# Kernel tuning notes

Hardware: AMD Instinct MI355X
Metric: run time of the kernel (lower is better)

Reference implementation:

```python
import jax, jax.numpy as jnp
import numpy as np

N, E, D = 100000, 1280000, 64


def setup_inputs() -> dict:
    key = jax.random.key(0)
    ks = jax.random.split(key, 9)
    x = jax.random.normal(ks[0], (N, D), jnp.float32)
    edge_index = jax.random.randint(ks[1], (2, E), 0, N, dtype=jnp.int64)
    edge_weight = jax.random.uniform(ks[2], (E,), jnp.float32)
    s = 1.0 / np.sqrt(D)
    W0 = jax.random.normal(ks[3], (D, D), jnp.float32) * s
    b0 = jnp.zeros((D,), jnp.float32)
    W1 = jax.random.normal(ks[4], (D, D), jnp.float32) * s
    b1 = jnp.zeros((D,), jnp.float32)
    W2 = jax.random.normal(ks[5], (D, D), jnp.float32) * s
    b2 = jnp.zeros((D,), jnp.float32)
    return {"x": x, "edge_index": edge_index, "edge_weight": edge_weight,
            "W0": W0, "b0": b0, "W1": W1, "b1": b1, "W2": W2, "b2": b2}


def reference(x, edge_index, edge_weight, W0, b0, W1, b1, W2, b2):
    n = x.shape[0]
    row, col = edge_index[0], edge_index[1]
    # GCN normalization with self-loops (PyG gcn_norm, fill_value=1)
    loop = jnp.arange(n)
    row_f = jnp.concatenate([row, loop])
    col_f = jnp.concatenate([col, loop])
    w_f = jnp.concatenate([edge_weight, jnp.ones((n,), x.dtype)])
    deg = jax.ops.segment_sum(w_f, col_f, num_segments=n)
    dinv = jnp.where(deg > 0, jax.lax.rsqrt(deg), 0.0).astype(x.dtype)
    norm = dinv[row_f] * w_f * dinv[col_f]  # [E+N]

    def conv(h, W, b):
        h = h @ W                                  # [N, D_out]
        msg = h[row_f] * norm[:, None]             # gather + scale
        return jax.ops.segment_sum(msg, col_f, num_segments=n) + b

    results = [x]
    h = jax.nn.relu(conv(x, W0, b0))   # dropout p=0 / eval -> identity
    results.append(h)
    h = jax.nn.relu(conv(h, W1, b1))
    results.append(h)
    h = conv(h, W2, b2)                # last layer: no activation
    results.append(h)
    return tuple(results)
```

## Files before the change

kernel.cpp:

```cpp
#include <hip/hip_runtime.h>
#include <hip/hip_fp16.h>


#define TPB 256
#define P1_CHUNK 4096
#define DSH 7
#define DNB 128
#define STAGE_CAP 4096

__global__ __launch_bounds__(TPB) void k_p0(const int* __restrict__ col,
                                            int* __restrict__ chist, int E, int nbk) {
    __shared__ int h[1024];
    int tid = threadIdx.x;
    for (int i = tid; i < nbk; i += TPB) h[i] = 0;
    __syncthreads();
    int s0 = blockIdx.x * P1_CHUNK;
    int s1 = min(s0 + P1_CHUNK, E);
    for (int i = s0 + tid; i < s1; i += TPB) atomicAdd(&h[col[i] >> DSH], 1);
    __syncthreads();
    for (int i = tid; i < nbk; i += TPB)
        if (h[i]) atomicAdd(&chist[i], h[i]);
}

__global__ __launch_bounds__(1024) void k_scanb(const int* __restrict__ chist,
                                                int* __restrict__ cbase,
                                                int* __restrict__ ccur, int nbk, int E) {
    __shared__ int s[1024];
    int tid = threadIdx.x;
    int v = (tid < nbk) ? chist[tid] : 0;
    s[tid] = v;
    __syncthreads();
    for (int off = 1; off < 1024; off <<= 1) {
        int t = (tid >= off) ? s[tid - off] : 0;
        __syncthreads();
        s[tid] += t;
        __syncthreads();
    }
    if (tid < nbk) { int ex = s[tid] - v; cbase[tid] = ex; ccur[tid] = ex; }
    if (tid == 0) cbase[nbk] = E;
}

__global__ __launch_bounds__(TPB) void k_p1(const int* __restrict__ row,
                                            const int* __restrict__ col,
                                            const float* __restrict__ w,
                                            int* __restrict__ ccur,
                                            int2* __restrict__ bkt, int E, int nbk) {
    __shared__ int h[1024];
    __shared__ int base[1024];
    int tid = threadIdx.x;
    for (int i = tid; i < nbk; i += TPB) h[i] = 0;
    __syncthreads();
    int s0 = blockIdx.x * P1_CHUNK;
    int s1 = min(s0 + P1_CHUNK, E);
    for (int i = s0 + tid; i < s1; i += TPB) atomicAdd(&h[col[i] >> DSH], 1);
    __syncthreads();
    for (int i = tid; i < nbk; i += TPB) {
        int c = h[i];
        base[i] = c ? atomicAdd(&ccur[i], c) : 0;
        h[i] = 0;
    }
    __syncthreads();
    for (int i = s0 + tid; i < s1; i += TPB) {
        int c = col[i];
        int b = c >> DSH;
        int r = atomicAdd(&h[b], 1);
        bkt[base[b] + r] = make_int2(row[i] | ((c & (DNB - 1)) << 20), __float_as_int(w[i]));
    }
}

__global__ __launch_bounds__(TPB) void k_p2(const int2* __restrict__ bkt,
                                            const int* __restrict__ cbase,
                                            int* __restrict__ starts,
                                            int2* __restrict__ edges,
                                            float* __restrict__ dinv, int n, int E) {
    __shared__ int hist[DNB];
    __shared__ int curs[DNB];
    __shared__ int sc[DNB];
    __shared__ int2 stage[STAGE_CAP];
    int tid = threadIdx.x;
    int b = blockIdx.x;
    int s0 = cbase[b], s1 = cbase[b + 1];
    int cnt = s1 - s0;
    int nodeBase = b << DSH;
    if (tid < DNB) hist[tid] = 0;
    __syncthreads();
    for (int i = s0 + tid; i < s1; i += TPB)
        atomicAdd(&hist[(unsigned)bkt[i].x >> 20], 1);
    __syncthreads();
    int v = 0;
    if (tid < DNB) { v = hist[tid]; sc[tid] = v; }
    __syncthreads();
    for (int off = 1; off < DNB; off <<= 1) {
        int t = 0;
        if (tid < DNB && tid >= off) t = sc[tid - off];
        __syncthreads();
        if (tid < DNB) sc[tid] += t;
        __syncthreads();
    }
    if (tid < DNB) {
        int ex = sc[tid] - v;
        curs[tid] = ex;
        int node = nodeBase + tid;
        if (node < n) starts[node] = s0 + ex;
    }
    if (b == 0 && tid == 0) starts[n] = E;
    __syncthreads();
    if (cnt <= STAGE_CAP) {
        for (int i = s0 + tid; i < s1; i += TPB) {
            int2 ed = bkt[i];
            int d = (unsigned)ed.x >> 20;
            int r = atomicAdd(&curs[d], 1);
            stage[r] = make_int2(ed.x & 0xFFFFF, ed.y);
        }
        __syncthreads();
        for (int i = tid; i < cnt; i += TPB) edges[s0 + i] = stage[i];
        if (tid < DNB) {
            int node = nodeBase + tid;
            if (node < n) {
                float d = 1.0f;
                for (int j = sc[tid] - v; j < sc[tid]; ++j)
                    d += __int_as_float(stage[j].y);
                dinv[node] = rsqrtf(d);
            }
        }
    } else {
        for (int i = s0 + tid; i < s1; i += TPB) {
            int2 ed = bkt[i];
            int d = (unsigned)ed.x >> 20;
            int r = atomicAdd(&curs[d], 1);
            edges[s0 + r] = make_int2(ed.x & 0xFFFFF, ed.y);
        }
        __syncthreads();
        if (tid < DNB) {
            int node = nodeBase + tid;
            if (node < n) {
                float d = 1.0f;
                for (int j = sc[tid] - v; j < sc[tid]; ++j)
                    d += __int_as_float(edges[s0 + j].y);
                dinv[node] = rsqrtf(d);
            }
        }
    }
}

__global__ __launch_bounds__(TPB, 3) void k_gemm64(const float* __restrict__ in,
                                                   const float* __restrict__ Wg,
                                                   __half* __restrict__ hwh,
                                                   const float* __restrict__ dinvg,
                                                   float* __restrict__ cp, int n) {
    __shared__ float4 Ws[1024];
    __shared__ float4 As[2048];
    int tid = threadIdx.x;
    const float4* Wf4 = (const float4*)Wg;
    #pragma unroll
    for (int i = 0; i < 4; ++i) Ws[i * 256 + tid] = Wf4[i * 256 + tid];
    int rowbase = blockIdx.x * 128;
    const float4* Af4 = (const float4*)in;
    #pragma unroll
    for (int i = 0; i < 8; ++i) {
        int f4 = i * 256 + tid;
        int r = f4 >> 4, c4 = f4 & 15;
        float4 v = make_float4(0.f, 0.f, 0.f, 0.f);
        if (rowbase + r < n) {
            v = Af4[(size_t)(rowbase + r) * 16 + c4];
            if (cp) *(float4*)&cp[((size_t)(rowbase + r) * 16 + c4) * 4] = v;
        }
        As[r * 16 + (c4 ^ ((r >> 3) & 3))] = v;
    }
    __syncthreads();
    int jg = tid & 15;
    int rg = tid >> 4;
    int r0 = rg * 8;
    int sw = rg & 3;
    float4 acc[8];
    #pragma unroll
    for (int rr = 0; rr < 8; ++rr) acc[rr] = make_float4(0.f, 0.f, 0.f, 0.f);
    #pragma unroll 2
    for (int kt = 0; kt < 16; ++kt) {
        float4 w0 = Ws[(kt * 4 + 0) * 16 + jg];
        float4 w1 = Ws[(kt * 4 + 1) * 16 + jg];
        float4 w2 = Ws[(kt * 4 + 2) * 16 + jg];
        float4 w3 = Ws[(kt * 4 + 3) * 16 + jg];
        int ac = kt ^ sw;
        #pragma unroll
        for (int rr = 0; rr < 8; ++rr) {
            float4 a = As[(r0 + rr) * 16 + ac];
            acc[rr].x = fmaf(a.x, w0.x, acc[rr].x);
            acc[rr].y = fmaf(a.x, w0.y, acc[rr].y);
            acc[rr].z = fmaf(a.x, w0.z, acc[rr].z);
            acc[rr].w = fmaf(a.x, w0.w, acc[rr].w);
            acc[rr].x = fmaf(a.y, w1.x, acc[rr].x);
            acc[rr].y = fmaf(a.y, w1.y, acc[rr].y);
            acc[rr].z = fmaf(a.y, w1.z, acc[rr].z);
            acc[rr].w = fmaf(a.y, w1.w, acc[rr].w);
            acc[rr].x = fmaf(a.z, w2.x, acc[rr].x);
            acc[rr].y = fmaf(a.z, w2.y, acc[rr].y);
            acc[rr].z = fmaf(a.z, w2.z, acc[rr].z);
            acc[rr].w = fmaf(a.z, w2.w, acc[rr].w);
            acc[rr].x = fmaf(a.w, w3.x, acc[rr].x);
            acc[rr].y = fmaf(a.w, w3.y, acc[rr].y);
            acc[rr].z = fmaf(a.w, w3.z, acc[rr].z);
            acc[rr].w = fmaf(a.w, w3.w, acc[rr].w);
        }
    }
    #pragma unroll
    for (int rr = 0; rr < 8; ++rr) {
        int r = rowbase + r0 + rr;
        if (r < n) {
            float di = dinvg[r];
            ushort4 s;
            s.x = __half_as_ushort(__float2half(acc[rr].x * di));
            s.y = __half_as_ushort(__float2half(acc[rr].y * di));
            s.z = __half_as_ushort(__float2half(acc[rr].z * di));
            s.w = __half_as_ushort(__float2half(acc[rr].w * di));
            *(ushort4*)&hwh[(size_t)r * 64 + jg * 4] = s;
        }
    }
}

__global__ __launch_bounds__(TPB) void k_gather(const int* __restrict__ starts,
                                                const int2* __restrict__ edges,
                                                const __half* __restrict__ hwh,
                                                const float* __restrict__ dinv,
                                                const float* __restrict__ b,
                                                float* __restrict__ out,
                                                int n, int relu) {
    int node = blockIdx.x * 4 + (threadIdx.x >> 6);
    if (node >= n) return;
    int lane = threadIdx.x & 63;
    int eslot = lane >> 4;
    int f = (lane & 15) << 2;
    int s0 = starts[node], s1 = starts[node + 1];
    float4 acc = make_float4(0.f, 0.f, 0.f, 0.f);
    const long long* epk = (const long long*)edges;
    int e = s0 + eslot;
    for (; e + 4 < s1; e += 8) {
        long long ev0 = __builtin_nontemporal_load(&epk[e]);
        long long ev1 = __builtin_nontemporal_load(&epk[e + 4]);
        ushort4 u0 = *(const ushort4*)&hwh[(size_t)(int)ev0 * 64 + f];
        ushort4 u1 = *(const ushort4*)&hwh[(size_t)(int)ev1 * 64 + f];
        float w0 = __int_as_float((int)(ev0 >> 32));
        float w1 = __int_as_float((int)(ev1 >> 32));
        acc.x = fmaf(__half2float(__ushort_as_half(u0.x)), w0, acc.x);
        acc.y = fmaf(__half2float(__ushort_as_half(u0.y)), w0, acc.y);
        acc.z = fmaf(__half2float(__ushort_as_half(u0.z)), w0, acc.z);
        acc.w = fmaf(__half2float(__ushort_as_half(u0.w)), w0, acc.w);
        acc.x = fmaf(__half2float(__ushort_as_half(u1.x)), w1, acc.x);
        acc.y = fmaf(__half2float(__ushort_as_half(u1.y)), w1, acc.y);
        acc.z = fmaf(__half2float(__ushort_as_half(u1.z)), w1, acc.z);
        acc.w = fmaf(__half2float(__ushort_as_half(u1.w)), w1, acc.w);
    }
    if (e < s1) {
        long long ev = __builtin_nontemporal_load(&epk[e]);
        ushort4 u = *(const ushort4*)&hwh[(size_t)(int)ev * 64 + f];
        float w = __int_as_float((int)(ev >> 32));
        acc.x = fmaf(__half2float(__ushort_as_half(u.x)), w, acc.x);
        acc.y = fmaf(__half2float(__ushort_as_half(u.y)), w, acc.y);
        acc.z = fmaf(__half2float(__ushort_as_half(u.z)), w, acc.z);
        acc.w = fmaf(__half2float(__ushort_as_half(u.w)), w, acc.w);
    }
    acc.x += __shfl_xor(acc.x, 16);
    acc.y += __shfl_xor(acc.y, 16);
    acc.z += __shfl_xor(acc.z, 16);
    acc.w += __shfl_xor(acc.w, 16);
    acc.x += __shfl_xor(acc.x, 32);
    acc.y += __shfl_xor(acc.y, 32);
    acc.z += __shfl_xor(acc.z, 32);
    acc.w += __shfl_xor(acc.w, 32);
    if (eslot == 0) {
        float di = dinv[node];
        ushort4 us = *(const ushort4*)&hwh[(size_t)node * 64 + f];
        float4 bb = *(const float4*)&b[f];
        float4 o;
        o.x = fmaf(__half2float(__ushort_as_half(us.x)) + acc.x, di, bb.x);
        o.y = fmaf(__half2float(__ushort_as_half(us.y)) + acc.y, di, bb.y);
        o.z = fmaf(__half2float(__ushort_as_half(us.z)) + acc.z, di, bb.z);
        o.w = fmaf(__half2float(__ushort_as_half(us.w)) + acc.w, di, bb.w);
        if (relu) {
            o.x = o.x > 0.f ? o.x : 0.f;
            o.y = o.y > 0.f ? o.y : 0.f;
            o.z = o.z > 0.f ? o.z : 0.f;
            o.w = o.w > 0.f ? o.w : 0.f;
        }
        *(float4*)&out[(size_t)node * 64 + f] = o;
    }
}

extern "C" void kernel_launch(void* const* d_in, const int* in_sizes, int n_in,
                              void* d_out, int out_size, void* d_ws, size_t ws_size,
                              hipStream_t stream) {
    const float* x = (const float*)d_in[0];
    const int* ei = (const int*)d_in[1];
    const float* ew = (const float*)d_in[2];
    const float* Wl[3] = {(const float*)d_in[3], (const float*)d_in[5], (const float*)d_in[7]};
    const float* Bl[3] = {(const float*)d_in[4], (const float*)d_in[6], (const float*)d_in[8]};

    const int n = in_sizes[0] / 64;
    const int E = in_sizes[2];
    const int* row = ei;
    const int* col = ei + E;
    float* out = (float*)d_out;

    const int nbk = (n + DNB - 1) >> DSH;
    const int p1b = (E + P1_CHUNK - 1) / P1_CHUNK;

    char* ws = (char*)d_ws;
    size_t o = 0;
    float* dinv  = (float*)(ws + o);  o = (o + (size_t)n * 4 + 255) & ~(size_t)255;
    __half* hwh  = (__half*)(ws + o);
    int2*  bkt   = (int2*)(ws + o);
    {
        size_t hb = (size_t)n * 128, bb = (size_t)E * 8;
        o = (o + (hb > bb ? hb : bb) + 255) & ~(size_t)255;
    }
    int* starts  = (int*)(ws + o);    o = (o + (size_t)(n + 1) * 4 + 255) & ~(size_t)255;
    int* chist   = (int*)(ws + o);    o = (o + 1024 * 4 + 255) & ~(size_t)255;
    int* cbase   = (int*)(ws + o);    o = (o + 1025 * 4 + 255) & ~(size_t)255;
    int* ccur    = (int*)(ws + o);    o = (o + 1024 * 4 + 255) & ~(size_t)255;
    int2* edges  = (int2*)(ws + o);

    hipMemsetAsync(chist, 0, (size_t)nbk * 4, stream);
    k_p0<<<p1b, TPB, 0, stream>>>(col, chist, E, nbk);
    k_scanb<<<1, 1024, 0, stream>>>(chist, cbase, ccur, nbk, E);
    k_p1<<<p1b, TPB, 0, stream>>>(row, col, ew, ccur, bkt, E, nbk);
    k_p2<<<nbk, TPB, 0, stream>>>(bkt, cbase, starts, edges, dinv, n, E);

    const float* hin = x;
    for (int L = 0; L < 3; ++L) {
        float* oseg = out + (size_t)(L + 1) * n * 64;
        k_gemm64<<<(n + 127) / 128, TPB, 0, stream>>>(hin, Wl[L], hwh, dinv, L == 0 ? out : nullptr, n);
        k_gather<<<(n + 3) / 4, TPB, 0, stream>>>(starts, edges, hwh, dinv, Bl[L], oseg, n, L < 2 ? 1 : 0);
        hin = oseg;
    }
}
```

Baseline: 424.4 us.

## Remap gather to one lane per feature with wave-uniform edge walk

The gather kernel changes from splitting each node's wave into four edge slots with four features per lane to one feature per lane, with every lane of the wave walking all edges. Edge index and weight loads become wave-uniform (node forced scalar via readfirstlane), the loop is unrolled by eight with power-of-two tails, and the cross-slot shuffle reduction is removed. This trades 8-byte vector feature loads for 2-byte per-lane loads, which still coalesce into one 128-byte row, in exchange for more edges in flight and no reduction. Nontemporal hints on the edge stream are also dropped.

```diff
diff --git a/kernel.cpp b/kernel.cpp
--- a/kernel.cpp
+++ b/kernel.cpp
@@ -225,65 +225,73 @@
                                                 const float* __restrict__ b,
                                                 float* __restrict__ out,
                                                 int n, int relu) {
-    int node = blockIdx.x * 4 + (threadIdx.x >> 6);
+    int node = __builtin_amdgcn_readfirstlane(blockIdx.x * (TPB / 64) + (threadIdx.x >> 6));
     if (node >= n) return;
     int lane = threadIdx.x & 63;
-    int eslot = lane >> 4;
-    int f = (lane & 15) << 2;
     int s0 = starts[node], s1 = starts[node + 1];
-    float4 acc = make_float4(0.f, 0.f, 0.f, 0.f);
     const long long* epk = (const long long*)edges;
-    int e = s0 + eslot;
-    for (; e + 4 < s1; e += 8) {
-        long long ev0 = __builtin_nontemporal_load(&epk[e]);
-        long long ev1 = __builtin_nontemporal_load(&epk[e + 4]);
-        ushort4 u0 = *(const ushort4*)&hwh[(size_t)(int)ev0 * 64 + f];
-        ushort4 u1 = *(const ushort4*)&hwh[(size_t)(int)ev1 * 64 + f];
-        float w0 = __int_as_float((int)(ev0 >> 32));
-        float w1 = __int_as_float((int)(ev1 >> 32));
-        acc.x = fmaf(__half2float(__ushort_as_half(u0.x)), w0, acc.x);
-        acc.y = fmaf(__half2float(__ushort_as_half(u0.y)), w0, acc.y);
-        acc.z = fmaf(__half2float(__ushort_as_half(u0.z)), w0, acc.z);
-        acc.w = fmaf(__half2float(__ushort_as_half(u0.w)), w0, acc.w);
-        acc.x = fmaf(__half2float(__ushort_as_half(u1.x)), w1, acc.x);
-        acc.y = fmaf(__half2float(__ushort_as_half(u1.y)), w1, acc.y);
-        acc.z = fmaf(__half2float(__ushort_as_half(u1.z)), w1, acc.z);
-        acc.w = fmaf(__half2float(__ushort_as_half(u1.w)), w1, acc.w);
+    float acc = 0.f;
+    int e = s0;
+    for (; e + 8 <= s1; e += 8) {
+        long long v0 = epk[e + 0];
+        long long v1 = epk[e + 1];
+        long long v2 = epk[e + 2];
+        long long v3 = epk[e + 3];
+        long long v4 = epk[e + 4];
+        long long v5 = epk[e + 5];
+        long long v6 = epk[e + 6];
+        long long v7 = epk[e + 7];
+        float h0 = __half2float(hwh[(size_t)(int)v0 * 64 + lane]);
+        float h1 = __half2float(hwh[(size_t)(int)v1 * 64 + lane]);
+        float h2 = __half2float(hwh[(size_t)(int)v2 * 64 + lane]);
+        float h3 = __half2float(hwh[(size_t)(int)v3 * 64 + lane]);
+        float h4 = __half2float(hwh[(size_t)(int)v4 * 64 + lane]);
+        float h5 = __half2float(hwh[(size_t)(int)v5 * 64 + lane]);
+        float h6 = __half2float(hwh[(size_t)(int)v6 * 64 + lane]);
+        float h7 = __half2float(hwh[(size_t)(int)v7 * 64 + lane]);
+        acc = fmaf(h0, __int_as_float((int)(v0 >> 32)), acc);
+        acc = fmaf(h1, __int_as_float((int)(v1 >> 32)), acc);
+        acc = fmaf(h2, __int_as_float((int)(v2 >> 32)), acc);
+        acc = fmaf(h3, __int_as_float((int)(v3 >> 32)), acc);
+        acc = fmaf(h4, __int_as_float((int)(v4 >> 32)), acc);
+        acc = fmaf(h5, __int_as_float((int)(v5 >> 32)), acc);
+        acc = fmaf(h6, __int_as_float((int)(v6 >> 32)), acc);
+        acc = fmaf(h7, __int_as_float((int)(v7 >> 32)), acc);
+    }
+    if (e + 4 <= s1) {
+        long long v0 = epk[e + 0];
+        long long v1 = epk[e + 1];
+        long long v2 = epk[e + 2];
+        long long v3 = epk[e + 3];
+        float h0 = __half2float(hwh[(size_t)(int)v0 * 64 + lane]);
+        float h1 = __half2float(hwh[(size_t)(int)v1 * 64 + lane]);
+        float h2 = __half2float(hwh[(size_t)(int)v2 * 64 + lane]);
+        float h3 = __half2float(hwh[(size_t)(int)v3 * 64 + lane]);
+        acc = fmaf(h0, __int_as_float((int)(v0 >> 32)), acc);
+        acc = fmaf(h1, __int_as_float((int)(v1 >> 32)), acc);
+        acc = fmaf(h2, __int_as_float((int)(v2 >> 32)), acc);
+        acc = fmaf(h3, __int_as_float((int)(v3 >> 32)), acc);
+        e += 4;
+    }
+    if (e + 2 <= s1) {
+        long long v0 = epk[e + 0];
+        long long v1 = epk[e + 1];
+        float h0 = __half2float(hwh[(size_t)(int)v0 * 64 + lane]);
+        float h1 = __half2float(hwh[(size_t)(int)v1 * 64 + lane]);
+        acc = fmaf(h0, __int_as_float((int)(v0 >> 32)), acc);
+        acc = fmaf(h1, __int_as_float((int)(v1 >> 32)), acc);
+        e += 2;
     }
     if (e < s1) {
-        long long ev = __builtin_nontemporal_load(&epk[e]);
-        ushort4 u = *(const ushort4*)&hwh[(size_t)(int)ev * 64 + f];
-        float w = __int_as_float((int)(ev >> 32));
-        acc.x = fmaf(__half2float(__ushort_as_half(u.x)), w, acc.x);
-        acc.y = fmaf(__half2float(__ushort_as_half(u.y)), w, acc.y);
-        acc.z = fmaf(__half2float(__ushort_as_half(u.z)), w, acc.z);
-        acc.w = fmaf(__half2float(__ushort_as_half(u.w)), w, acc.w);
-    }
-    acc.x += __shfl_xor(acc.x, 16);
-    acc.y += __shfl_xor(acc.y, 16);
-    acc.z += __shfl_xor(acc.z, 16);
-    acc.w += __shfl_xor(acc.w, 16);
-    acc.x += __shfl_xor(acc.x, 32);
-    acc.y += __shfl_xor(acc.y, 32);
-    acc.z += __shfl_xor(acc.z, 32);
-    acc.w += __shfl_xor(acc.w, 32);
-    if (eslot == 0) {
-        float di = dinv[node];
-        ushort4 us = *(const ushort4*)&hwh[(size_t)node * 64 + f];
-        float4 bb = *(const float4*)&b[f];
-        float4 o;
-        o.x = fmaf(__half2float(__ushort_as_half(us.x)) + acc.x, di, bb.x);
-        o.y = fmaf(__half2float(__ushort_as_half(us.y)) + acc.y, di, bb.y);
-        o.z = fmaf(__half2float(__ushort_as_half(us.z)) + acc.z, di, bb.z);
-        o.w = fmaf(__half2float(__ushort_as_half(us.w)) + acc.w, di, bb.w);
-        if (relu) {
-            o.x = o.x > 0.f ? o.x : 0.f;
-            o.y = o.y > 0.f ? o.y : 0.f;
-            o.z = o.z > 0.f ? o.z : 0.f;
-            o.w = o.w > 0.f ? o.w : 0.f;
-        }
-        *(float4*)&out[(size_t)node * 64 + f] = o;
-    }
+        long long v0 = epk[e];
+        float h0 = __half2float(hwh[(size_t)(int)v0 * 64 + lane]);
+        acc = fmaf(h0, __int_as_float((int)(v0 >> 32)), acc);
+    }
+    float di = dinv[node];
+    float self = __half2float(hwh[(size_t)node * 64 + lane]);
+    float o = fmaf(self + acc, di, b[lane]);
+    if (relu) o = o > 0.f ? o : 0.f;
+    out[(size_t)node * 64 + lane] = o;
 }
 
 extern "C" void kernel_launch(void* const* d_in, const int* in_sizes, int n_in,
@@ -329,7 +337,7 @@
     for (int L = 0; L < 3; ++L) {
         float* oseg = out + (size_t)(L + 1) * n * 64;
         k_gemm64<<<(n + 127) / 128, TPB, 0, stream>>>(hin, Wl[L], hwh, dinv, L == 0 ? out : nullptr, n);
-        k_gather<<<(n + 3) / 4, TPB, 0, stream>>>(starts, edges, hwh, dinv, Bl[L], oseg, n, L < 2 ? 1 : 0);
+        k_gather<<<(n * 64 + TPB - 1) / TPB, TPB, 0, stream>>>(starts, edges, hwh, dinv, Bl[L], oseg, n, L < 2 ? 1 : 0);
         hin = oseg;
     }
 }
```

After: 368.8 us. 1.15x faster.
